# Kernel tuning notes

Measured on AMD Instinct MI355X. Metric: run time of the kernel, lower is better.

## Reference

```python
import jax, jax.numpy as jnp
import numpy as np
from math import sqrt

D_MODEL = 1024
N_HEADS = 16
E = D_MODEL // N_HEADS  # d_keys = d_values = 64


def setup_inputs() -> dict:
    key = jax.random.key(0)
    ks = jax.random.split(key, 11)
    B, L, S = 2, 2048, 2048
    s = 1.0 / sqrt(D_MODEL)
    return {
        "queries": jax.random.normal(ks[0], (B, L, D_MODEL), jnp.float32),
        "keys": jax.random.normal(ks[1], (B, S, D_MODEL), jnp.float32),
        "values": jax.random.normal(ks[2], (B, S, D_MODEL), jnp.float32),
        "Wq": jax.random.normal(ks[3], (D_MODEL, D_MODEL), jnp.float32) * s,
        "bq": jnp.zeros((D_MODEL,), jnp.float32),
        "Wk": jax.random.normal(ks[4], (D_MODEL, D_MODEL), jnp.float32) * s,
        "bk": jnp.zeros((D_MODEL,), jnp.float32),
        "Wv": jax.random.normal(ks[5], (D_MODEL, D_MODEL), jnp.float32) * s,
        "bv": jnp.zeros((D_MODEL,), jnp.float32),
        "Wo": jax.random.normal(ks[6], (D_MODEL, D_MODEL), jnp.float32) * s,
        "bo": jnp.zeros((D_MODEL,), jnp.float32),
    }


def reference(queries, keys, values, Wq, bq, Wk, bk, Wv, bv, Wo, bo):
    B, L, _ = queries.shape
    S = keys.shape[1]
    H = N_HEADS
    # projections -> [B, L/S, H, E]
    q = (queries @ Wq + bq).reshape(B, L, H, E)
    k = (keys @ Wk + bk).reshape(B, S, H, E)
    v = (values @ Wv + bv).reshape(B, S, H, E)
    scale = 1.0 / sqrt(E)
    scores = jnp.einsum('blhe,bshe->bhls', q, k)  # [B,H,L,S]
    A = jax.nn.softmax(scale * scores, axis=-1)   # dropout = identity (eval)
    V = jnp.einsum('bhls,bshd->blhd', A, v)       # [B,L,H,E]
    out = V.reshape(B, L, H * E) @ Wo + bo
    return out
```

## Files before the change

### kernel.cpp

```cpp
#include <hip/hip_runtime.h>
#include <hip/hip_bf16.h>
#include <stdint.h>

#define BATCH 2
#define SEQ   2048
#define DM    1024
#define NH    16
#define EH    64
#define MROWS (BATCH*SEQ)

typedef __attribute__((ext_vector_type(8))) short  short8;
typedef __attribute__((ext_vector_type(4))) float  floatx4;
typedef __attribute__((ext_vector_type(8))) unsigned short ushort8v;
typedef __attribute__((ext_vector_type(4))) unsigned short ushort4v;

__device__ __forceinline__ unsigned short f2bf(float f) {
    return (unsigned short)((__float_as_uint(f) + 0x8000u) >> 16);
}

__device__ __forceinline__ void gload_lds16(const void* g, void* l) {
    __builtin_amdgcn_global_load_lds(
        (const __attribute__((address_space(1))) unsigned int*)g,
        (__attribute__((address_space(3))) unsigned int*)l, 16, 0, 0);
}

__global__ __launch_bounds__(256)
void transpose_w(const float* __restrict__ W0, const float* __restrict__ W1,
                 const float* __restrict__ W2, const float* __restrict__ W3,
                 unsigned short* __restrict__ T0, unsigned short* __restrict__ T1,
                 unsigned short* __restrict__ T2, unsigned short* __restrict__ T3,
                 int zbase)
{
    int z = zbase + blockIdx.z;
    const float* W = (z == 0) ? W0 : (z == 1) ? W1 : (z == 2) ? W2 : W3;
    unsigned short* T = (z == 0) ? T0 : (z == 1) ? T1 : (z == 2) ? T2 : T3;
    __shared__ float t[32][33];
    const int tid = threadIdx.x;
    const int k0 = blockIdx.y * 32, n0 = blockIdx.x * 32;
    {
        int r = tid >> 3, c4 = (tid & 7) * 4;
        float4 u = *(const float4*)&W[(size_t)(k0 + r) * DM + n0 + c4];
        t[r][c4 + 0] = u.x; t[r][c4 + 1] = u.y; t[r][c4 + 2] = u.z; t[r][c4 + 3] = u.w;
    }
    __syncthreads();
    {
        int n = tid >> 3, k4 = (tid & 7) * 4;
        ushort4v o;
        o[0] = f2bf(t[k4 + 0][n]); o[1] = f2bf(t[k4 + 1][n]);
        o[2] = f2bf(t[k4 + 2][n]); o[3] = f2bf(t[k4 + 3][n]);
        *(ushort4v*)&T[(size_t)(n0 + n) * DM + k0 + k4] = o;
    }
}

struct ProjArgs {
    const float* act[3];
    const unsigned short* wt[3];
    const float* bias[3];
    unsigned short* C[3];
    float oscale[3];
};

__global__ __launch_bounds__(256)
void proj_qkv(ProjArgs pa)
{
    const int z = blockIdx.z;
    const bool vt = (z == 2);
    const int linear = (int)(blockIdx.x + gridDim.x * blockIdx.y);
    int rb, cb;
    if (!vt) { rb = linear & 31; cb = linear >> 5; }
    else     { cb = linear & 31; rb = linear >> 5; }
    const int row0 = rb * 128, col0 = cb * 128;

    const float* act = pa.act[z];
    const unsigned short* wt = pa.wt[z];
    const int actBase = vt ? col0 : row0;
    const int wtBase  = vt ? row0 : col0;

    __shared__ unsigned short As[128 * 64];
    __shared__ unsigned short Bs[128 * 64];
    unsigned short* conv = vt ? Bs : As;
    unsigned short* wdst = vt ? As : Bs;

    const int tid = threadIdx.x;
    const int lane = tid & 63, w = tid >> 6;
    const int lane15 = lane & 15, quad = lane >> 4;
    const int wr = (w >> 1) * 64, wc = (w & 1) * 64;

    floatx4 acc[4][4] = {};

    const int ar = tid >> 1, kh = tid & 1;
    float4 pre[8];

    auto loadPre = [&](int kt) {
        const float* p = &act[(size_t)(actBase + ar) * DM + kt + kh * 32];
#pragma unroll
        for (int j = 0; j < 8; ++j) pre[j] = ((const float4*)p)[j];
    };
    auto cvtStore = [&]() {
#pragma unroll
        for (int j = 0; j < 4; ++j) {
            int c = kh * 4 + j;
            int slot = c ^ (ar & 7);
            float4 u0 = pre[2 * j], u1 = pre[2 * j + 1];
            ushort8v o8;
            o8[0] = f2bf(u0.x); o8[1] = f2bf(u0.y); o8[2] = f2bf(u0.z); o8[3] = f2bf(u0.w);
            o8[4] = f2bf(u1.x); o8[5] = f2bf(u1.y); o8[6] = f2bf(u1.z); o8[7] = f2bf(u1.w);
            *(ushort8v*)&conv[(size_t)(ar * 8 + slot) * 8] = o8;
        }
    };
    auto stageW = [&](int kt) {
#pragma unroll
        for (int rr = 0; rr < 4; ++rr) {
            int p = rr * 256 + w * 64 + lane;
            int row = p >> 3;
            int gch = (p & 7) ^ (row & 7);
            gload_lds16(&wt[(size_t)(wtBase + row) * DM + kt + gch * 8],
                        (char*)wdst + (size_t)(rr * 256 + w * 64) * 16);
        }
    };

    loadPre(0);
    for (int kt = 0; kt < DM; kt += 64) {
        __syncthreads();
        stageW(kt);
        cvtStore();
        __syncthreads();
        if (kt + 64 < DM) loadPre(kt + 64);

        short8 af[4][2], bf[4][2];
#pragma unroll
        for (int i = 0; i < 4; ++i) {
            int row = wr + i * 16 + lane15;
#pragma unroll
            for (int ks = 0; ks < 2; ++ks)
                af[i][ks] = *(const short8*)&As[(size_t)(row * 8 +
                                (((ks << 2) + quad) ^ (lane15 & 7))) * 8];
        }
#pragma unroll
        for (int j = 0; j < 4; ++j) {
            int row = wc + j * 16 + lane15;
#pragma unroll
            for (int ks = 0; ks < 2; ++ks)
                bf[j][ks] = *(const short8*)&Bs[(size_t)(row * 8 +
                                (((ks << 2) + quad) ^ (lane15 & 7))) * 8];
        }
#pragma unroll
        for (int i = 0; i < 4; ++i)
#pragma unroll
            for (int j = 0; j < 4; ++j)
#pragma unroll
                for (int ks = 0; ks < 2; ++ks)
                    acc[i][j] = __builtin_amdgcn_mfma_f32_16x16x32_bf16(
                        af[i][ks], bf[j][ks], acc[i][j], 0, 0, 0);
    }

    const float* bias = pa.bias[z];
    const float os = pa.oscale[z];
    unsigned short* C = pa.C[z];
#pragma unroll
    for (int i = 0; i < 4; ++i) {
#pragma unroll
        for (int j = 0; j < 4; ++j) {
#pragma unroll
            for (int r = 0; r < 4; ++r) {
                int row = row0 + wr + i * 16 + quad * 4 + r;
                int col = col0 + wc + j * 16 + lane15;
                if (!vt) {
                    float v = (acc[i][j][r] + bias[col]) * os;
                    int b = row >> 11, l = row & (SEQ - 1);
                    int h = col >> 6,  e = col & (EH - 1);
                    C[((size_t)(b * NH + h) * SEQ + l) * EH + e] = f2bf(v);
                } else {
                    float v = acc[i][j][r] + bias[row];
                    int h = row >> 6,  e = row & (EH - 1);
                    int b = col >> 11, l = col & (SEQ - 1);
                    C[((size_t)(b * NH + h) * EH + e) * SEQ + l] = f2bf(v);
                }
            }
        }
    }
}

__global__ __launch_bounds__(256)
void gemm_out(const unsigned short* __restrict__ ctx,
              const unsigned short* __restrict__ WoT,
              const float* __restrict__ bo,
              float* __restrict__ out)
{
    const int linear = (int)(blockIdx.x + gridDim.x * blockIdx.y);
    const int rb = linear & 31, cb = linear >> 5;
    const int row0 = rb * 128, col0 = cb * 64;

    __shared__ unsigned short As[128 * 64];
    __shared__ unsigned short Bs[64 * 64];

    const int tid = threadIdx.x;
    const int lane = tid & 63, w = tid >> 6;
    const int lane15 = lane & 15, quad = lane >> 4;
    const int wr = (w >> 1) * 64, wc = (w & 1) * 32;

    floatx4 acc[4][2] = {};

    auto stageA = [&](int kt) {
#pragma unroll
        for (int rr = 0; rr < 4; ++rr) {
            int p = rr * 256 + w * 64 + lane;
            int row = p >> 3, gch = (p & 7) ^ (row & 7);
            gload_lds16(&ctx[(size_t)(row0 + row) * DM + kt + gch * 8],
                        (char*)As + (size_t)(rr * 256 + w * 64) * 16);
        }
    };
    auto stageB = [&](int kt) {
#pragma unroll
        for (int rr = 0; rr < 2; ++rr) {
            int p = rr * 256 + w * 64 + lane;
            int row = p >> 3, gch = (p & 7) ^ (row & 7);
            gload_lds16(&WoT[(size_t)(col0 + row) * DM + kt + gch * 8],
                        (char*)Bs + (size_t)(rr * 256 + w * 64) * 16);
        }
    };

    for (int kt = 0; kt < DM; kt += 64) {
        __syncthreads();
        stageA(kt);
        stageB(kt);
        __syncthreads();

        short8 af[4][2], bf[2][2];
#pragma unroll
        for (int i = 0; i < 4; ++i) {
            int row = wr + i * 16 + lane15;
#pragma unroll
            for (int ks = 0; ks < 2; ++ks)
                af[i][ks] = *(const short8*)&As[(size_t)(row * 8 +
                                (((ks << 2) + quad) ^ (lane15 & 7))) * 8];
        }
#pragma unroll
        for (int j = 0; j < 2; ++j) {
            int row = wc + j * 16 + lane15;
#pragma unroll
            for (int ks = 0; ks < 2; ++ks)
                bf[j][ks] = *(const short8*)&Bs[(size_t)(row * 8 +
                                (((ks << 2) + quad) ^ (lane15 & 7))) * 8];
        }
#pragma unroll
        for (int i = 0; i < 4; ++i)
#pragma unroll
            for (int j = 0; j < 2; ++j)
#pragma unroll
                for (int ks = 0; ks < 2; ++ks)
                    acc[i][j] = __builtin_amdgcn_mfma_f32_16x16x32_bf16(
                        af[i][ks], bf[j][ks], acc[i][j], 0, 0, 0);
    }

#pragma unroll
    for (int i = 0; i < 4; ++i)
#pragma unroll
        for (int j = 0; j < 2; ++j)
#pragma unroll
            for (int r = 0; r < 4; ++r) {
                int row = row0 + wr + i * 16 + quad * 4 + r;
                int col = col0 + wc + j * 16 + lane15;
                out[(size_t)row * DM + col] = acc[i][j][r] + bo[col];
            }
}

__device__ __forceinline__ void stage_kv(const unsigned short* __restrict__ Kp,
                                         const unsigned short* __restrict__ Vp,
                                         int st, unsigned short* ksb, unsigned short* vsb,
                                         int w, int lane)
{
#pragma unroll
    for (int rr = 0; rr < 2; ++rr) {
        int p = rr * 256 + w * 64 + lane;
        int row = p >> 3;
        int gch = (p & 7) ^ (row & 7);
        gload_lds16(&Kp[(size_t)(st + row) * EH + gch * 8],
                    ksb + (size_t)(rr * 256 + w * 64) * 8);
        gload_lds16(&Vp[(size_t)row * SEQ + st + gch * 8],
                    vsb + (size_t)(rr * 256 + w * 64) * 8);
    }
}

__global__ __launch_bounds__(256)
void attn_mfma(const unsigned short* __restrict__ Qh,
               const unsigned short* __restrict__ Kh,
               const unsigned short* __restrict__ Vt,
               unsigned short* __restrict__ ctx)
{
    __shared__ unsigned short Ks[2][64 * 64];
    __shared__ unsigned short Vs[2][64 * 64];
    __shared__ unsigned short Ps[128][72];

    const int tid = threadIdx.x;
    const int lane = tid & 63, w = tid >> 6;
    const int lane15 = lane & 15, quad = lane >> 4;

    const int linear = (int)(blockIdx.x + 16 * (blockIdx.y + 16 * blockIdx.z));
    const int bhid = linear & 31;
    const int qt = linear >> 5;
    const int h = bhid & 15, b = bhid >> 4;

    const size_t bh = (size_t)(b * NH + h);
    const unsigned short* Kp = Kh + bh * SEQ * EH;
    const unsigned short* Vp = Vt + bh * EH * SEQ;

    short8 qf[2][2];
    {
        const unsigned short* Qp =
            Qh + (bh * SEQ + (size_t)qt * 128 + w * 32 + lane15) * EH;
#pragma unroll
        for (int ks = 0; ks < 2; ++ks) {
            qf[0][ks] = *(const short8*)(Qp + ks * 32 + quad * 8);
            qf[1][ks] = *(const short8*)(Qp + 16 * EH + ks * 32 + quad * 8);
        }
    }
    short8 ones;
#pragma unroll
    for (int i = 0; i < 8; ++i) ones[i] = (short)0x3F80;

    floatx4 o[2][4] = {};
    floatx4 lacc[2] = {};

    stage_kv(Kp, Vp, 0, Ks[0], Vs[0], w, lane);
    __syncthreads();
    int cur = 0;

    for (int st = 0; st < SEQ; st += 64) {
        int nxt = cur ^ 1;
        if (st + 64 < SEQ)
            stage_kv(Kp, Vp, st + 64, Ks[nxt], Vs[nxt], w, lane);
        const unsigned short* ksb = Ks[cur];
        const unsigned short* vsb = Vs[cur];

        floatx4 sacc[4][2] = {};
#pragma unroll
        for (int ts = 0; ts < 4; ++ts) {
#pragma unroll
            for (int ks = 0; ks < 2; ++ks) {
                short8 kf = *(const short8*)&ksb[((ts * 16 + lane15) << 6) +
                                                 ((((ks << 2) + quad) ^ (lane15 & 7)) << 3)];
                sacc[ts][0] = __builtin_amdgcn_mfma_f32_16x16x32_bf16(kf, qf[0][ks], sacc[ts][0], 0, 0, 0);
                sacc[ts][1] = __builtin_amdgcn_mfma_f32_16x16x32_bf16(kf, qf[1][ks], sacc[ts][1], 0, 0, 0);
            }
        }

#pragma unroll
        for (int ts = 0; ts < 4; ++ts)
#pragma unroll
            for (int nq = 0; nq < 2; ++nq) {
                unsigned int u0 = __float_as_uint(__builtin_amdgcn_exp2f(sacc[ts][nq][0])) + 0x8000u;
                unsigned int u1 = __float_as_uint(__builtin_amdgcn_exp2f(sacc[ts][nq][1])) + 0x8000u;
                unsigned int u2 = __float_as_uint(__builtin_amdgcn_exp2f(sacc[ts][nq][2])) + 0x8000u;
                unsigned int u3 = __float_as_uint(__builtin_amdgcn_exp2f(sacc[ts][nq][3])) + 0x8000u;
                uint2 pk;
                pk.x = (u0 >> 16) | (u1 & 0xFFFF0000u);
                pk.y = (u2 >> 16) | (u3 & 0xFFFF0000u);
                *(uint2*)&Ps[w * 32 + nq * 16 + lane15][ts * 16 + quad * 4] = pk;
            }

#pragma unroll
        for (int ks = 0; ks < 2; ++ks) {
            short8 pf[2];
#pragma unroll
            for (int mt = 0; mt < 2; ++mt) {
                pf[mt] = *(const short8*)&Ps[w * 32 + mt * 16 + lane15][ks * 32 + quad * 8];
                lacc[mt] = __builtin_amdgcn_mfma_f32_16x16x32_bf16(pf[mt], ones, lacc[mt], 0, 0, 0);
            }
#pragma unroll
            for (int t2 = 0; t2 < 4; ++t2) {
                short8 vf = *(const short8*)&vsb[((t2 * 16 + lane15) << 6) +
                                                 ((((ks << 2) + quad) ^ (lane15 & 7)) << 3)];
                o[0][t2] = __builtin_amdgcn_mfma_f32_16x16x32_bf16(pf[0], vf, o[0][t2], 0, 0, 0);
                o[1][t2] = __builtin_amdgcn_mfma_f32_16x16x32_bf16(pf[1], vf, o[1][t2], 0, 0, 0);
            }
        }
        __syncthreads();
        cur = nxt;
    }

#pragma unroll
    for (int mt = 0; mt < 2; ++mt) {
        float inv[4];
#pragma unroll
        for (int r = 0; r < 4; ++r) inv[r] = 1.0f / lacc[mt][r];
#pragma unroll
        for (int t2 = 0; t2 < 4; ++t2)
#pragma unroll
            for (int r = 0; r < 4; ++r) {
                int q = qt * 128 + w * 32 + mt * 16 + quad * 4 + r;
                int col = h * EH + t2 * 16 + lane15;
                ctx[((size_t)(b * SEQ + q)) * DM + col] = f2bf(o[mt][t2][r] * inv[r]);
            }
    }
}

extern "C" void kernel_launch(void* const* d_in, const int* in_sizes, int n_in,
                              void* d_out, int out_size, void* d_ws, size_t ws_size,
                              hipStream_t stream)
{
    const float* queries = (const float*)d_in[0];
    const float* keys    = (const float*)d_in[1];
    const float* values  = (const float*)d_in[2];
    const float* Wq = (const float*)d_in[3];
    const float* bq = (const float*)d_in[4];
    const float* Wk = (const float*)d_in[5];
    const float* bk = (const float*)d_in[6];
    const float* Wv = (const float*)d_in[7];
    const float* bv = (const float*)d_in[8];
    const float* Wo = (const float*)d_in[9];
    const float* bo = (const float*)d_in[10];
    float* out = (float*)d_out;

    unsigned short* ws = (unsigned short*)d_ws;
    const size_t MAT = (size_t)MROWS * DM;
    const size_t WSZ = (size_t)DM * DM;
    unsigned short* Qhp = ws;
    unsigned short* Khp = ws + MAT;
    unsigned short* Vtp = ws + 2 * MAT;
    unsigned short* ctx = ws + 3 * MAT;
    unsigned short* WqT = ctx;
    unsigned short* WkT = ctx + WSZ;
    unsigned short* WvT = ctx + 2 * WSZ;
    unsigned short* WoT = ws;

    const float qscale = 0.125f * 1.44269504088896f;

    transpose_w<<<dim3(DM / 32, DM / 32, 3), 256, 0, stream>>>(
        Wq, Wk, Wv, Wo, WqT, WkT, WvT, WoT, 0);

    ProjArgs pa;
    pa.act[0] = queries; pa.act[1] = keys; pa.act[2] = values;
    pa.wt[0] = WqT;      pa.wt[1] = WkT;   pa.wt[2] = WvT;
    pa.bias[0] = bq;     pa.bias[1] = bk;  pa.bias[2] = bv;
    pa.C[0] = Qhp;       pa.C[1] = Khp;    pa.C[2] = Vtp;
    pa.oscale[0] = qscale; pa.oscale[1] = 1.f; pa.oscale[2] = 1.f;
    proj_qkv<<<dim3(8, 32, 3), 256, 0, stream>>>(pa);

    attn_mfma<<<dim3(SEQ / 128, NH, BATCH), 256, 0, stream>>>(Qhp, Khp, Vtp, ctx);

    transpose_w<<<dim3(DM / 32, DM / 32, 1), 256, 0, stream>>>(
        Wq, Wk, Wv, Wo, WqT, WkT, WvT, WoT, 3);

    gemm_out<<<dim3(16, 32), 256, 0, stream>>>(ctx, WoT, bo, out);
}
```

Measured before the change: 268.0 us.

## Reshape GEMM warp tiling to row-strips and swizzle attention P buffer

The projection and output GEMMs now give each wave a 32-row strip spanning the full block width (2x8 and 2x4 MFMA tiles) instead of a 2x2 quadrant layout. K-steps are processed one at a time to cut fragment register pressure. Activation loads are reorganised so 8 consecutive threads read contiguous 32-byte chunks of a row, which should improve coalescing, and the convert-store is issued before the async weight staging. The attention P scratch buffer drops its padding in favour of an XOR swizzle to avoid LDS bank conflicts while saving shared memory; the trade-off is that the 32-row strips re-read all B fragments per wave, raising LDS read traffic.

```diff
diff --git a/kernel.cpp b/kernel.cpp
--- a/kernel.cpp
+++ b/kernel.cpp
@@ -78,34 +78,38 @@
 
     __shared__ unsigned short As[128 * 64];
     __shared__ unsigned short Bs[128 * 64];
-    unsigned short* conv = vt ? Bs : As;
-    unsigned short* wdst = vt ? As : Bs;
+    unsigned short* convDst  = vt ? Bs : As;
+    unsigned short* asyncDst = vt ? As : Bs;
 
     const int tid = threadIdx.x;
     const int lane = tid & 63, w = tid >> 6;
     const int lane15 = lane & 15, quad = lane >> 4;
-    const int wr = (w >> 1) * 64, wc = (w & 1) * 64;
-
-    floatx4 acc[4][4] = {};
-
-    const int ar = tid >> 1, kh = tid & 1;
+
+    floatx4 acc[2][8] = {};
+
+    const int arow0 = tid >> 3;
+    const int cno   = tid & 7;
+    const int acol  = cno * 8;
+
     float4 pre[8];
-
     auto loadPre = [&](int kt) {
-        const float* p = &act[(size_t)(actBase + ar) * DM + kt + kh * 32];
-#pragma unroll
-        for (int j = 0; j < 8; ++j) pre[j] = ((const float4*)p)[j];
+#pragma unroll
+        for (int q = 0; q < 4; ++q) {
+            const float* p = &act[(size_t)(actBase + q * 32 + arow0) * DM + kt + acol];
+            pre[q * 2]     = *(const float4*)p;
+            pre[q * 2 + 1] = *(const float4*)(p + 4);
+        }
     };
     auto cvtStore = [&]() {
 #pragma unroll
-        for (int j = 0; j < 4; ++j) {
-            int c = kh * 4 + j;
-            int slot = c ^ (ar & 7);
-            float4 u0 = pre[2 * j], u1 = pre[2 * j + 1];
+        for (int q = 0; q < 4; ++q) {
+            int row  = q * 32 + arow0;
+            int slot = cno ^ (row & 7);
+            float4 u0 = pre[q * 2], u1 = pre[q * 2 + 1];
             ushort8v o8;
             o8[0] = f2bf(u0.x); o8[1] = f2bf(u0.y); o8[2] = f2bf(u0.z); o8[3] = f2bf(u0.w);
             o8[4] = f2bf(u1.x); o8[5] = f2bf(u1.y); o8[6] = f2bf(u1.z); o8[7] = f2bf(u1.w);
-            *(ushort8v*)&conv[(size_t)(ar * 8 + slot) * 8] = o8;
+            *(ushort8v*)&convDst[(size_t)(row * 8 + slot) * 8] = o8;
         }
     };
     auto stageW = [&](int kt) {
@@ -115,56 +119,53 @@
             int row = p >> 3;
             int gch = (p & 7) ^ (row & 7);
             gload_lds16(&wt[(size_t)(wtBase + row) * DM + kt + gch * 8],
-                        (char*)wdst + (size_t)(rr * 256 + w * 64) * 16);
+                        (char*)asyncDst + (size_t)(rr * 256 + w * 64) * 16);
         }
     };
 
     loadPre(0);
     for (int kt = 0; kt < DM; kt += 64) {
         __syncthreads();
+        cvtStore();
         stageW(kt);
-        cvtStore();
         __syncthreads();
         if (kt + 64 < DM) loadPre(kt + 64);
 
-        short8 af[4][2], bf[4][2];
-#pragma unroll
-        for (int i = 0; i < 4; ++i) {
-            int row = wr + i * 16 + lane15;
-#pragma unroll
-            for (int ks = 0; ks < 2; ++ks)
-                af[i][ks] = *(const short8*)&As[(size_t)(row * 8 +
-                                (((ks << 2) + quad) ^ (lane15 & 7))) * 8];
-        }
-#pragma unroll
-        for (int j = 0; j < 4; ++j) {
-            int row = wc + j * 16 + lane15;
-#pragma unroll
-            for (int ks = 0; ks < 2; ++ks)
-                bf[j][ks] = *(const short8*)&Bs[(size_t)(row * 8 +
-                                (((ks << 2) + quad) ^ (lane15 & 7))) * 8];
-        }
-#pragma unroll
-        for (int i = 0; i < 4; ++i)
-#pragma unroll
-            for (int j = 0; j < 4; ++j)
-#pragma unroll
-                for (int ks = 0; ks < 2; ++ks)
+#pragma unroll
+        for (int ks = 0; ks < 2; ++ks) {
+            short8 af[2], bf[8];
+#pragma unroll
+            for (int i = 0; i < 2; ++i) {
+                int row = w * 32 + i * 16 + lane15;
+                af[i] = *(const short8*)&As[(size_t)(row * 8 +
+                            (((ks << 2) + quad) ^ (row & 7))) * 8];
+            }
+#pragma unroll
+            for (int j = 0; j < 8; ++j) {
+                int row = j * 16 + lane15;
+                bf[j] = *(const short8*)&Bs[(size_t)(row * 8 +
+                            (((ks << 2) + quad) ^ (row & 7))) * 8];
+            }
+#pragma unroll
+            for (int i = 0; i < 2; ++i)
+#pragma unroll
+                for (int j = 0; j < 8; ++j)
                     acc[i][j] = __builtin_amdgcn_mfma_f32_16x16x32_bf16(
-                        af[i][ks], bf[j][ks], acc[i][j], 0, 0, 0);
+                        af[i], bf[j], acc[i][j], 0, 0, 0);
+        }
     }
 
     const float* bias = pa.bias[z];
     const float os = pa.oscale[z];
     unsigned short* C = pa.C[z];
 #pragma unroll
-    for (int i = 0; i < 4; ++i) {
-#pragma unroll
-        for (int j = 0; j < 4; ++j) {
+    for (int i = 0; i < 2; ++i) {
+#pragma unroll
+        for (int j = 0; j < 8; ++j) {
 #pragma unroll
             for (int r = 0; r < 4; ++r) {
-                int row = row0 + wr + i * 16 + quad * 4 + r;
-                int col = col0 + wc + j * 16 + lane15;
+                int row = row0 + w * 32 + i * 16 + quad * 4 + r;
+                int col = col0 + j * 16 + lane15;
                 if (!vt) {
                     float v = (acc[i][j][r] + bias[col]) * os;
                     int b = row >> 11, l = row & (SEQ - 1);
@@ -197,9 +198,8 @@
     const int tid = threadIdx.x;
     const int lane = tid & 63, w = tid >> 6;
     const int lane15 = lane & 15, quad = lane >> 4;
-    const int wr = (w >> 1) * 64, wc = (w & 1) * 32;
-
-    floatx4 acc[4][2] = {};
+
+    floatx4 acc[2][4] = {};
 
     auto stageA = [&](int kt) {
 #pragma unroll
@@ -226,41 +226,38 @@
         stageB(kt);
         __syncthreads();
 
-        short8 af[4][2], bf[2][2];
-#pragma unroll
-        for (int i = 0; i < 4; ++i) {
-            int row = wr + i * 16 + lane15;
-#pragma unroll
-            for (int ks = 0; ks < 2; ++ks)
-                af[i][ks] = *(const short8*)&As[(size_t)(row * 8 +
-                                (((ks << 2) + quad) ^ (lane15 & 7))) * 8];
-        }
-#pragma unroll
-        for (int j = 0; j < 2; ++j) {
-            int row = wc + j * 16 + lane15;
-#pragma unroll
-            for (int ks = 0; ks < 2; ++ks)
-                bf[j][ks] = *(const short8*)&Bs[(size_t)(row * 8 +
-                                (((ks << 2) + quad) ^ (lane15 & 7))) * 8];
-        }
-#pragma unroll
-        for (int i = 0; i < 4; ++i)
-#pragma unroll
-            for (int j = 0; j < 2; ++j)
-#pragma unroll
-                for (int ks = 0; ks < 2; ++ks)
+#pragma unroll
+        for (int ks = 0; ks < 2; ++ks) {
+            short8 af[2], bf[4];
+#pragma unroll
+            for (int i = 0; i < 2; ++i) {
+                int row = w * 32 + i * 16 + lane15;
+                af[i] = *(const short8*)&As[(size_t)(row * 8 +
+                            (((ks << 2) + quad) ^ (row & 7))) * 8];
+            }
+#pragma unroll
+            for (int j = 0; j < 4; ++j) {
+                int row = j * 16 + lane15;
+                bf[j] = *(const short8*)&Bs[(size_t)(row * 8 +
+                            (((ks << 2) + quad) ^ (row & 7))) * 8];
+            }
+#pragma unroll
+            for (int i = 0; i < 2; ++i)
+#pragma unroll
+                for (int j = 0; j < 4; ++j)
                     acc[i][j] = __builtin_amdgcn_mfma_f32_16x16x32_bf16(
-                        af[i][ks], bf[j][ks], acc[i][j], 0, 0, 0);
-    }
-
-#pragma unroll
-    for (int i = 0; i < 4; ++i)
-#pragma unroll
-        for (int j = 0; j < 2; ++j)
+                        af[i], bf[j], acc[i][j], 0, 0, 0);
+        }
+    }
+
+#pragma unroll
+    for (int i = 0; i < 2; ++i)
+#pragma unroll
+        for (int j = 0; j < 4; ++j)
 #pragma unroll
             for (int r = 0; r < 4; ++r) {
-                int row = row0 + wr + i * 16 + quad * 4 + r;
-                int col = col0 + wc + j * 16 + lane15;
+                int row = row0 + w * 32 + i * 16 + quad * 4 + r;
+                int col = col0 + j * 16 + lane15;
                 out[(size_t)row * DM + col] = acc[i][j][r] + bo[col];
             }
 }
@@ -290,7 +287,7 @@
 {
     __shared__ unsigned short Ks[2][64 * 64];
     __shared__ unsigned short Vs[2][64 * 64];
-    __shared__ unsigned short Ps[128][72];
+    __shared__ unsigned short Ps[128][64];
 
     const int tid = threadIdx.x;
     const int lane = tid & 63, w = tid >> 6;
@@ -356,7 +353,8 @@
                 uint2 pk;
                 pk.x = (u0 >> 16) | (u1 & 0xFFFF0000u);
                 pk.y = (u2 >> 16) | (u3 & 0xFFFF0000u);
-                *(uint2*)&Ps[w * 32 + nq * 16 + lane15][ts * 16 + quad * 4] = pk;
+                *(uint2*)&Ps[w * 32 + nq * 16 + lane15]
+                            [(((ts * 2 + (quad >> 1)) ^ (lane15 & 7)) << 3) + ((quad & 1) << 2)] = pk;
             }
 
 #pragma unroll
@@ -364,7 +362,8 @@
             short8 pf[2];
 #pragma unroll
             for (int mt = 0; mt < 2; ++mt) {
-                pf[mt] = *(const short8*)&Ps[w * 32 + mt * 16 + lane15][ks * 32 + quad * 8];
+                pf[mt] = *(const short8*)&Ps[w * 32 + mt * 16 + lane15]
+                                            [((((ks << 2) + quad) ^ (lane15 & 7)) << 3)];
                 lacc[mt] = __builtin_amdgcn_mfma_f32_16x16x32_bf16(pf[mt], ones, lacc[mt], 0, 0, 0);
             }
 #pragma unroll
```

Result: faster. 238.6 us (-11.0%).
